# Kernel optimization log

Measured on AMD Instinct MI355X. Metric: run time of the kernel, lower is better.

## Reference

```python
import jax, jax.numpy as jnp
import numpy as np

N_NODES = 50000
N_EDGES = 800000
D = 128
E_DIM = 32
N_LAYERS = 4
BN_EPS = 1e-5


def setup_inputs() -> dict:
    key = jax.random.key(0)
    ks = jax.random.split(key, 9)
    return {
        "x": jax.random.normal(ks[0], (N_NODES, D), dtype=jnp.float32),
        "edge_attr": jax.random.normal(ks[1], (N_EDGES, E_DIM), dtype=jnp.float32),
        "edge_index": jax.random.randint(ks[2], (2, N_EDGES), 0, N_NODES, dtype=jnp.int64),
        "W_edge": jax.random.normal(ks[3], (N_LAYERS, E_DIM, D), dtype=jnp.float32) * 0.1,
        "b_edge": jnp.zeros((N_LAYERS, D), dtype=jnp.float32),
        "W1": jax.random.normal(ks[4], (N_LAYERS, D, D), dtype=jnp.float32) * 0.1,
        "b1": jnp.zeros((N_LAYERS, D), dtype=jnp.float32),
        "W2": jax.random.normal(ks[5], (N_LAYERS, D, D), dtype=jnp.float32) * 0.1,
        "b2": jnp.zeros((N_LAYERS, D), dtype=jnp.float32),
        "gamma": jnp.ones((N_LAYERS, D), dtype=jnp.float32),
        "beta": jnp.zeros((N_LAYERS, D), dtype=jnp.float32),
    }


def reference(x, edge_attr, edge_index, W_edge, b_edge, W1, b1, W2, b2, gamma, beta):
    src, dst = edge_index[0], edge_index[1]
    n = x.shape[0]
    for i in range(N_LAYERS):
        # GINEConv: message = ReLU(x_src + Lin(edge_attr)); scatter-add to dst
        e = edge_attr @ W_edge[i] + b_edge[i]            # [E, D]
        m = jax.nn.relu(x[src] + e)                      # [E, D]
        agg = jax.ops.segment_sum(m, dst, num_segments=n)  # [N, D]
        h = x + agg                                      # (1+eps)*x, eps=0
        # 2-layer MLP
        h = jax.nn.relu(h @ W1[i] + b1[i]) @ W2[i] + b2[i]
        # BatchNorm (training-mode batch stats, biased var) + ReLU; dropout off
        mean = h.mean(axis=0)
        var = h.var(axis=0)
        h = (h - mean) * jax.lax.rsqrt(var + BN_EPS) * gamma[i] + beta[i]
        x = jax.nn.relu(h)
    return x
```

## Files before the change

### kernel.cpp

```cpp
#include <hip/hip_runtime.h>

#define NN 50000
#define NE 800000
#define DD 128
#define ED 32
#define NL 4
#define BN_EPS 1e-5f
#define SCAN_B 1024
#define NB ((NN + SCAN_B - 1) / SCAN_B)
#define EB 128
#define MR 32

typedef __attribute__((ext_vector_type(8))) short bf16x8;
typedef __attribute__((ext_vector_type(4))) float f32x4;

__device__ __forceinline__ unsigned short f2bf(float f) {
    unsigned u = __float_as_uint(f);
    u += 0x7fffu + ((u >> 16) & 1u);
    return (unsigned short)(u >> 16);
}
__device__ __forceinline__ float bf2f(unsigned short h) {
    return __uint_as_float((unsigned)h << 16);
}

__global__ __launch_bounds__(256) void hist_kernel(
    const int* __restrict__ edst, int* __restrict__ deg)
{
    const int e = blockIdx.x * 256 + threadIdx.x;
    if (e < NE) atomicAdd(&deg[edst[e]], 1);
}

__global__ __launch_bounds__(256) void scan1_kernel(
    const int* __restrict__ deg, int* __restrict__ rowptr, int* __restrict__ bsum)
{
    __shared__ int sh[256];
    const int t = threadIdx.x, b = blockIdx.x;
    const int base = b * SCAN_B + t * 4;
    int v[4];
#pragma unroll
    for (int j = 0; j < 4; ++j) {
        const int idx = base + j;
        v[j] = (idx < NN) ? deg[idx] : 0;
    }
    sh[t] = v[0] + v[1] + v[2] + v[3];
    __syncthreads();
    for (int off = 1; off < 256; off <<= 1) {
        const int val = (t >= off) ? sh[t - off] : 0;
        __syncthreads();
        sh[t] += val;
        __syncthreads();
    }
    int p = (t == 0) ? 0 : sh[t - 1];
#pragma unroll
    for (int j = 0; j < 4; ++j) {
        const int idx = base + j;
        if (idx < NN) rowptr[idx] = p;
        p += v[j];
    }
    if (t == 255) bsum[b] = sh[255];
}

__global__ void scan2_kernel(int* __restrict__ bsum)
{
    if (threadIdx.x == 0) {
        int acc = 0;
        for (int i = 0; i < NB; ++i) { const int v = bsum[i]; bsum[i] = acc; acc += v; }
    }
}

__global__ __launch_bounds__(256) void scan3_kernel(
    int* __restrict__ rowptr, int* __restrict__ cursor, const int* __restrict__ bsum)
{
    const int idx = blockIdx.x * 256 + threadIdx.x;
    if (idx < NN) {
        const int v = rowptr[idx] + bsum[idx / SCAN_B];
        rowptr[idx] = v;
        cursor[idx] = v;
    }
    if (idx == 0) rowptr[NN] = NE;
}

__global__ __launch_bounds__(256) void scatter_idx_kernel(
    const int* __restrict__ esrc, const int* __restrict__ edst,
    int* __restrict__ cursor, int2* __restrict__ sd_perm, int* __restrict__ eid_perm)
{
    const int e = blockIdx.x * 256 + threadIdx.x;
    if (e < NE) {
        const int d = edst[e];
        const int pos = atomicAdd(&cursor[d], 1);
        sd_perm[pos] = make_int2(esrc[e], d);
        eid_perm[pos] = e;
    }
}

__global__ __launch_bounds__(256) void ea_gather_kernel(
    const float* __restrict__ ea, const int* __restrict__ eid_perm,
    unsigned short* __restrict__ ea_bf)
{
    const int tid = blockIdx.x * 256 + threadIdx.x;
    const int pos = tid >> 3, j = tid & 7;
    if (pos < NE) {
        const int e = eid_perm[pos];
        const float4 v = *(const float4*)&ea[(size_t)e * ED + j * 4];
        uint2 p;
        p.x = (unsigned)f2bf(v.x) | ((unsigned)f2bf(v.y) << 16);
        p.y = (unsigned)f2bf(v.z) | ((unsigned)f2bf(v.w) << 16);
        *(uint2*)&ea_bf[(size_t)pos * ED + j * 4] = p;
    }
}

__global__ __launch_bounds__(256) void x0conv_kernel(
    const float* __restrict__ x0, unsigned short* __restrict__ xbf)
{
    const size_t i = ((size_t)blockIdx.x * 256 + threadIdx.x) * 8;
    if (i >= (size_t)NN * DD) return;
    const float4 a = *(const float4*)&x0[i];
    const float4 b = *(const float4*)&x0[i + 4];
    uint4 o;
    o.x = (unsigned)f2bf(a.x) | ((unsigned)f2bf(a.y) << 16);
    o.y = (unsigned)f2bf(a.z) | ((unsigned)f2bf(a.w) << 16);
    o.z = (unsigned)f2bf(b.x) | ((unsigned)f2bf(b.y) << 16);
    o.w = (unsigned)f2bf(b.z) | ((unsigned)f2bf(b.w) << 16);
    *(uint4*)&xbf[i] = o;
}

__global__ __launch_bounds__(256) void wconv_kernel(
    const float* __restrict__ We, unsigned short* __restrict__ wtb)
{
    const int tid = blockIdx.x * 256 + threadIdx.x;
    if (tid < NL * DD * ED) {
        const int l = tid / (DD * ED);
        const int r = tid % (DD * ED);
        const int c = r / ED, k = r % ED;
        wtb[tid] = f2bf(We[(size_t)l * ED * DD + k * DD + c]);
    }
}

__global__ __launch_bounds__(256) void w12conv_kernel(
    const float* __restrict__ W1, const float* __restrict__ W2,
    unsigned short* __restrict__ w1t, unsigned short* __restrict__ w2t)
{
    const int tid = blockIdx.x * 256 + threadIdx.x;
    if (tid < NL * DD * DD) {
        const int l = tid / (DD * DD);
        const int r = tid % (DD * DD);
        const int n = r / DD, k = r % DD;
        const size_t s = (size_t)l * DD * DD + k * DD + n;
        w1t[tid] = f2bf(W1[s]);
        w2t[tid] = f2bf(W2[s]);
    }
}

__global__ __launch_bounds__(256, 5) void edge_mfma_kernel(
    const unsigned short* __restrict__ xbf,
    const unsigned short* __restrict__ eab,
    const int2* __restrict__ sd_perm,
    const unsigned short* __restrict__ wtb,
    const float* __restrict__ be,
    float* __restrict__ agg)
{
    __shared__ unsigned short msgl[EB * 128];
    const int t = threadIdx.x;
    const int wv = t >> 6, ln = t & 63;
    const int l15 = ln & 15, kb = ln >> 4;
    const int e0 = blockIdx.x * EB;

    const int c0 = (2 * wv + 0) * 16 + l15;
    const int c1 = (2 * wv + 1) * 16 + l15;
    const bf16x8 bfr0 = *(const bf16x8*)&wtb[c0 * ED + kb * 8];
    const bf16x8 bfr1 = *(const bf16x8*)&wtb[c1 * ED + kb * 8];

#pragma unroll
    for (int eg = 0; eg < EB / 16; ++eg) {
        const int edge = eg * 16 + l15;
        const bf16x8 afr = *(const bf16x8*)&eab[(size_t)(e0 + edge) * ED + kb * 8];
        f32x4 z = {0.f, 0.f, 0.f, 0.f};
        const f32x4 d0 = __builtin_amdgcn_mfma_f32_16x16x32_bf16(afr, bfr0, z, 0, 0, 0);
        const f32x4 d1 = __builtin_amdgcn_mfma_f32_16x16x32_bf16(afr, bfr1, z, 0, 0, 0);
#pragma unroll
        for (int j = 0; j < 4; ++j) {
            const int mrow = eg * 16 + kb * 4 + j;
            const int sw = ((mrow >> 2) & 3) << 3;
            const int i0 = (((c0 >> 1) ^ sw) << 1) | (c0 & 1);
            const int i1 = (((c1 >> 1) ^ sw) << 1) | (c1 & 1);
            msgl[mrow * 128 + i0] = f2bf(d0[j]);
            msgl[mrow * 128 + i1] = f2bf(d1[j]);
        }
    }
    __syncthreads();

    const int lbase = wv * 32;
    const int2* sdp = &sd_perm[e0 + lbase];
    const int c2 = ln * 2;
    const float2 bv = *(const float2*)&be[c2];
    float2 acc = {0.f, 0.f};
    int seg_start = 0;
#pragma unroll 1
    for (int g = 0; g < 4; ++g) {
        const int gb = g * 8;
        int4 pr[4];
#pragma unroll
        for (int q = 0; q < 4; ++q)
            pr[q] = *(const int4*)&sdp[gb + 2 * q];
        const int srcs[8] = {pr[0].x, pr[0].z, pr[1].x, pr[1].z,
                             pr[2].x, pr[2].z, pr[3].x, pr[3].z};
        int dsts[9];
        dsts[0] = pr[0].y; dsts[1] = pr[0].w; dsts[2] = pr[1].y; dsts[3] = pr[1].w;
        dsts[4] = pr[2].y; dsts[5] = pr[2].w; dsts[6] = pr[3].y; dsts[7] = pr[3].w;
        dsts[8] = (gb + 8 < 32) ? sdp[gb + 8].y : -1;
        float2 xv[8];
#pragma unroll
        for (int q = 0; q < 8; ++q) {
            const unsigned xu = *(const unsigned*)&xbf[(size_t)srcs[q] * DD + c2];
            xv[q].x = __uint_as_float(xu << 16);
            xv[q].y = __uint_as_float(xu & 0xffff0000u);
        }
#pragma unroll
        for (int q = 0; q < 8; ++q) {
            const int i = gb + q;
            const int dw = ln ^ (((i >> 2) & 3) << 3);
            const unsigned mm = *(const unsigned*)&msgl[(lbase + i) * 128 + dw * 2];
            const float mlo = __uint_as_float(mm << 16);
            const float mhi = __uint_as_float(mm & 0xffff0000u);
            acc.x += fmaxf(xv[q].x + mlo + bv.x, 0.f);
            acc.y += fmaxf(xv[q].y + mhi + bv.y, 0.f);
            if (i == 31 || dsts[q + 1] != dsts[q]) {
                float* ap = &agg[(size_t)dsts[q] * DD + c2];
                if (seg_start > 0 && i < 31) {
                    *(float2*)ap = acc;
                } else {
                    unsafeAtomicAdd(ap + 0, acc.x);
                    unsafeAtomicAdd(ap + 1, acc.y);
                }
                acc.x = 0.f; acc.y = 0.f;
                seg_start = i + 1;
            }
        }
    }
}

__global__ __launch_bounds__(256, 5) void mlp_mfma_kernel(
    const unsigned short* __restrict__ xbf, const float* __restrict__ agg,
    float* __restrict__ h2out,
    const unsigned short* __restrict__ w1t,
    const unsigned short* __restrict__ w2t,
    const float* __restrict__ b1, const float* __restrict__ b2,
    float* __restrict__ bns)
{
    __shared__ unsigned short ah[MR * 128];
    __shared__ unsigned short al[MR * 128];
    __shared__ unsigned short bh[MR * 128];
    __shared__ unsigned short bl[MR * 128];
    const int t = threadIdx.x;
    const int wv = t >> 6, ln = t & 63, l15 = ln & 15, kb = ln >> 4;
    const int r0 = blockIdx.x * MR;

#pragma unroll
    for (int p = 0; p < 2; ++p) {
        const int row = p * 16 + (t >> 4);
        const int gc = t & 15;
        const int grow = r0 + row;
        float v[8] = {0.f, 0.f, 0.f, 0.f, 0.f, 0.f, 0.f, 0.f};
        if (grow < NN) {
            const size_t g = (size_t)grow * DD + gc * 8;
            const uint4 xu = *(const uint4*)&xbf[g];
            const float4 ga = *(const float4*)&agg[g];
            const float4 gb4 = *(const float4*)&agg[g + 4];
            v[0] = __uint_as_float(xu.x << 16)          + ga.x;
            v[1] = __uint_as_float(xu.x & 0xffff0000u)  + ga.y;
            v[2] = __uint_as_float(xu.y << 16)          + ga.z;
            v[3] = __uint_as_float(xu.y & 0xffff0000u)  + ga.w;
            v[4] = __uint_as_float(xu.z << 16)          + gb4.x;
            v[5] = __uint_as_float(xu.z & 0xffff0000u)  + gb4.y;
            v[6] = __uint_as_float(xu.w << 16)          + gb4.z;
            v[7] = __uint_as_float(xu.w & 0xffff0000u)  + gb4.w;
        }
        unsigned hiw[4], low[4];
#pragma unroll
        for (int j = 0; j < 4; ++j) {
            const unsigned short h0 = f2bf(v[2 * j]);
            const unsigned short h1 = f2bf(v[2 * j + 1]);
            const unsigned short q0 = f2bf(v[2 * j] - bf2f(h0));
            const unsigned short q1 = f2bf(v[2 * j + 1] - bf2f(h1));
            hiw[j] = (unsigned)h0 | ((unsigned)h1 << 16);
            low[j] = (unsigned)q0 | ((unsigned)q1 << 16);
        }
        const int off = row * 128 + (gc ^ (row & 7)) * 8;
        *(uint4*)&ah[off] = *(uint4*)hiw;
        *(uint4*)&al[off] = *(uint4*)low;
    }

    bf16x8 w1f[2][4];
#pragma unroll
    for (int nt = 0; nt < 2; ++nt) {
        const int n = wv * 32 + nt * 16 + l15;
#pragma unroll
        for (int ks = 0; ks < 4; ++ks)
            w1f[nt][ks] = *(const bf16x8*)&w1t[n * DD + ks * 32 + kb * 8];
    }
    const int cA = wv * 32 + l15, cB = wv * 32 + 16 + l15;
    const float b1v[2] = {b1[cA], b1[cB]};
    const float b2v[2] = {b2[cA], b2[cB]};
    __syncthreads();

    f32x4 acc[2][2];
#pragma unroll
    for (int mt = 0; mt < 2; ++mt)
#pragma unroll
        for (int nt = 0; nt < 2; ++nt)
            acc[mt][nt] = (f32x4){0.f, 0.f, 0.f, 0.f};
#pragma unroll
    for (int ks = 0; ks < 4; ++ks) {
#pragma unroll
        for (int mt = 0; mt < 2; ++mt) {
            const int row = mt * 16 + l15;
            const int off = row * 128 + ((ks * 4 + kb) ^ (row & 7)) * 8;
            const bf16x8 afh = *(const bf16x8*)&ah[off];
            const bf16x8 afl = *(const bf16x8*)&al[off];
#pragma unroll
            for (int nt = 0; nt < 2; ++nt) {
                acc[mt][nt] = __builtin_amdgcn_mfma_f32_16x16x32_bf16(afh, w1f[nt][ks], acc[mt][nt], 0, 0, 0);
                acc[mt][nt] = __builtin_amdgcn_mfma_f32_16x16x32_bf16(afl, w1f[nt][ks], acc[mt][nt], 0, 0, 0);
            }
        }
    }

#pragma unroll
    for (int mt = 0; mt < 2; ++mt) {
#pragma unroll
        for (int nt = 0; nt < 2; ++nt) {
            const int col = wv * 32 + nt * 16 + l15;
#pragma unroll
            for (int j = 0; j < 4; ++j) {
                const int row = mt * 16 + kb * 4 + j;
                const float v = fmaxf(acc[mt][nt][j] + b1v[nt], 0.f);
                const unsigned short hi = f2bf(v);
                const int off = row * 128 + ((col >> 3) ^ (row & 7)) * 8 + (col & 7);
                bh[off] = hi;
                bl[off] = f2bf(v - bf2f(hi));
            }
        }
    }

    bf16x8 w2f[2][4];
#pragma unroll
    for (int nt = 0; nt < 2; ++nt) {
        const int n = wv * 32 + nt * 16 + l15;
#pragma unroll
        for (int ks = 0; ks < 4; ++ks)
            w2f[nt][ks] = *(const bf16x8*)&w2t[n * DD + ks * 32 + kb * 8];
    }
    __syncthreads();

#pragma unroll
    for (int mt = 0; mt < 2; ++mt)
#pragma unroll
        for (int nt = 0; nt < 2; ++nt)
            acc[mt][nt] = (f32x4){0.f, 0.f, 0.f, 0.f};
#pragma unroll
    for (int ks = 0; ks < 4; ++ks) {
#pragma unroll
        for (int mt = 0; mt < 2; ++mt) {
            const int row = mt * 16 + l15;
            const int off = row * 128 + ((ks * 4 + kb) ^ (row & 7)) * 8;
            const bf16x8 afh = *(const bf16x8*)&bh[off];
            const bf16x8 afl = *(const bf16x8*)&bl[off];
#pragma unroll
            for (int nt = 0; nt < 2; ++nt) {
                acc[mt][nt] = __builtin_amdgcn_mfma_f32_16x16x32_bf16(afh, w2f[nt][ks], acc[mt][nt], 0, 0, 0);
                acc[mt][nt] = __builtin_amdgcn_mfma_f32_16x16x32_bf16(afl, w2f[nt][ks], acc[mt][nt], 0, 0, 0);
            }
        }
    }

    float ps[2] = {0.f, 0.f}, pq[2] = {0.f, 0.f};
#pragma unroll
    for (int mt = 0; mt < 2; ++mt) {
#pragma unroll
        for (int nt = 0; nt < 2; ++nt) {
            const int col = wv * 32 + nt * 16 + l15;
#pragma unroll
            for (int j = 0; j < 4; ++j) {
                const int row = r0 + mt * 16 + kb * 4 + j;
                const float v = acc[mt][nt][j] + b2v[nt];
                if (row < NN) {
                    h2out[(size_t)row * DD + col] = v;
                    ps[nt] += v;
                    pq[nt] += v * v;
                }
            }
        }
    }
#pragma unroll
    for (int nt = 0; nt < 2; ++nt) {
        ps[nt] += __shfl_xor(ps[nt], 16);
        ps[nt] += __shfl_xor(ps[nt], 32);
        pq[nt] += __shfl_xor(pq[nt], 16);
        pq[nt] += __shfl_xor(pq[nt], 32);
    }
    if (kb == 0) {
#pragma unroll
        for (int nt = 0; nt < 2; ++nt) {
            const int col = wv * 32 + nt * 16 + l15;
            unsafeAtomicAdd(&bns[col], ps[nt]);
            unsafeAtomicAdd(&bns[DD + col], pq[nt]);
        }
    }
}

__global__ __launch_bounds__(256) void bn_apply_bf16(
    const float* __restrict__ h2, const float* __restrict__ bns,
    const float* __restrict__ gamma, const float* __restrict__ beta,
    unsigned short* __restrict__ xout)
{
    const size_t i = ((size_t)blockIdx.x * 256 + threadIdx.x) * 4;
    if (i >= (size_t)NN * DD) return;
    const int c4 = (int)(i & 127);
    const float4 hv = *(const float4*)&h2[i];
    const float4 sv = *(const float4*)&bns[c4];
    const float4 qv = *(const float4*)&bns[DD + c4];
    const float4 gv = *(const float4*)&gamma[c4];
    const float4 bv = *(const float4*)&beta[c4];
    const float inv_n = 1.f / (float)NN;
    float o0, o1, o2, o3;
    { const float m = sv.x * inv_n; const float var = qv.x * inv_n - m * m;
      o0 = fmaxf((hv.x - m) * __frsqrt_rn(var + BN_EPS) * gv.x + bv.x, 0.f); }
    { const float m = sv.y * inv_n; const float var = qv.y * inv_n - m * m;
      o1 = fmaxf((hv.y - m) * __frsqrt_rn(var + BN_EPS) * gv.y + bv.y, 0.f); }
    { const float m = sv.z * inv_n; const float var = qv.z * inv_n - m * m;
      o2 = fmaxf((hv.z - m) * __frsqrt_rn(var + BN_EPS) * gv.z + bv.z, 0.f); }
    { const float m = sv.w * inv_n; const float var = qv.w * inv_n - m * m;
      o3 = fmaxf((hv.w - m) * __frsqrt_rn(var + BN_EPS) * gv.w + bv.w, 0.f); }
    uint2 o;
    o.x = (unsigned)f2bf(o0) | ((unsigned)f2bf(o1) << 16);
    o.y = (unsigned)f2bf(o2) | ((unsigned)f2bf(o3) << 16);
    *(uint2*)&xout[i] = o;
}

__global__ __launch_bounds__(256) void bn_apply_f32(
    const float* __restrict__ h2, const float* __restrict__ bns,
    const float* __restrict__ gamma, const float* __restrict__ beta,
    float* __restrict__ xout)
{
    const size_t i = ((size_t)blockIdx.x * 256 + threadIdx.x) * 4;
    if (i >= (size_t)NN * DD) return;
    const int c4 = (int)(i & 127);
    const float4 hv = *(const float4*)&h2[i];
    const float4 sv = *(const float4*)&bns[c4];
    const float4 qv = *(const float4*)&bns[DD + c4];
    const float4 gv = *(const float4*)&gamma[c4];
    const float4 bv = *(const float4*)&beta[c4];
    const float inv_n = 1.f / (float)NN;
    float4 ov;
    { const float m = sv.x * inv_n; const float var = qv.x * inv_n - m * m;
      ov.x = fmaxf((hv.x - m) * __frsqrt_rn(var + BN_EPS) * gv.x + bv.x, 0.f); }
    { const float m = sv.y * inv_n; const float var = qv.y * inv_n - m * m;
      ov.y = fmaxf((hv.y - m) * __frsqrt_rn(var + BN_EPS) * gv.y + bv.y, 0.f); }
    { const float m = sv.z * inv_n; const float var = qv.z * inv_n - m * m;
      ov.z = fmaxf((hv.z - m) * __frsqrt_rn(var + BN_EPS) * gv.z + bv.z, 0.f); }
    { const float m = sv.w * inv_n; const float var = qv.w * inv_n - m * m;
      ov.w = fmaxf((hv.w - m) * __frsqrt_rn(var + BN_EPS) * gv.w + bv.w, 0.f); }
    *(float4*)&xout[i] = ov;
}

extern "C" void kernel_launch(void* const* d_in, const int* in_sizes, int n_in,
                              void* d_out, int out_size, void* d_ws, size_t ws_size,
                              hipStream_t stream) {
    const float* x0    = (const float*)d_in[0];
    const float* ea    = (const float*)d_in[1];
    const int*   eidx  = (const int*)d_in[2];
    const float* We    = (const float*)d_in[3];
    const float* be    = (const float*)d_in[4];
    const float* W1    = (const float*)d_in[5];
    const float* b1    = (const float*)d_in[6];
    const float* W2    = (const float*)d_in[7];
    const float* b2    = (const float*)d_in[8];
    const float* gamma = (const float*)d_in[9];
    const float* beta  = (const float*)d_in[10];
    float* out = (float*)d_out;
    float* ws  = (float*)d_ws;

    float* agg = ws;
    float* bns = agg + (size_t)NN * DD;
    int* deg      = (int*)(bns + 256);
    int* rowptr   = deg + 50000;
    int* cursor   = rowptr + 50004;
    int* bsum     = cursor + 50000;
    int2* sd_perm = (int2*)(bsum + 64);
    int* eid_perm = (int*)(sd_perm + NE);
    unsigned short* ea_bf = (unsigned short*)(eid_perm + NE);
    unsigned short* wt_bf = ea_bf + (size_t)NE * ED;
    unsigned short* w1t   = wt_bf + (size_t)NL * DD * ED;
    unsigned short* w2t   = w1t + (size_t)NL * DD * DD;
    unsigned short* xbf   = w2t + (size_t)NL * DD * DD;

    const int* esrc = eidx;
    const int* edst = eidx + NE;

    hipMemsetAsync(deg, 0, NN * sizeof(int), stream);
    hist_kernel<<<(NE + 255) / 256, 256, 0, stream>>>(edst, deg);
    scan1_kernel<<<NB, 256, 0, stream>>>(deg, rowptr, bsum);
    scan2_kernel<<<1, 64, 0, stream>>>(bsum);
    scan3_kernel<<<(NN + 255) / 256, 256, 0, stream>>>(rowptr, cursor, bsum);
    scatter_idx_kernel<<<(NE + 255) / 256, 256, 0, stream>>>(
        esrc, edst, cursor, sd_perm, eid_perm);
    ea_gather_kernel<<<(NE * 8 + 255) / 256, 256, 0, stream>>>(ea, eid_perm, ea_bf);
    x0conv_kernel<<<((NN * DD / 8) + 255) / 256, 256, 0, stream>>>(x0, xbf);
    wconv_kernel<<<(NL * DD * ED + 255) / 256, 256, 0, stream>>>(We, wt_bf);
    w12conv_kernel<<<(NL * DD * DD + 255) / 256, 256, 0, stream>>>(W1, W2, w1t, w2t);

    for (int l = 0; l < NL; ++l) {
        hipMemsetAsync(agg, 0, (size_t)NN * DD * sizeof(float), stream);
        hipMemsetAsync(bns, 0, 2 * DD * sizeof(float), stream);
        edge_mfma_kernel<<<NE / EB, 256, 0, stream>>>(
            xbf, ea_bf, sd_perm,
            wt_bf + (size_t)l * DD * ED, be + (size_t)l * DD, agg);
        mlp_mfma_kernel<<<(NN + MR - 1) / MR, 256, 0, stream>>>(
            xbf, agg, agg,
            w1t + (size_t)l * DD * DD, w2t + (size_t)l * DD * DD,
            b1 + (size_t)l * DD, b2 + (size_t)l * DD, bns);
        if (l < NL - 1) {
            bn_apply_bf16<<<(NN * DD / 4 + 255) / 256, 256, 0, stream>>>(
                agg, bns, gamma + (size_t)l * DD, beta + (size_t)l * DD, xbf);
        } else {
            bn_apply_f32<<<(NN * DD / 4 + 255) / 256, 256, 0, stream>>>(
                agg, bns, gamma + (size_t)l * DD, beta + (size_t)l * DD, out);
        }
    }
}
```

Before: 669.7 us.

## Fold agg zeroing into BN apply, deterministic sd_perm fill, wider gather batches

The per-layer memset of the aggregation buffer is replaced by having bn_apply_bf16 write zeros back to h2 after reading it, and the BN stats get one slot per layer so they are cleared once up front. The scatter kernel now only writes eid_perm; a new per-node kernel fills sd_perm from rowptr so its writes are sequential. The edge kernel gathers 16 source rows per batch instead of 8 to put more loads in flight. The costs are one extra small kernel launch, a serial per-node loop in sdfill, and higher register pressure in the edge kernel.

```diff
diff --git a/kernel.cpp b/kernel.cpp
--- a/kernel.cpp
+++ b/kernel.cpp
@@ -81,15 +81,24 @@
 }
 
 __global__ __launch_bounds__(256) void scatter_idx_kernel(
-    const int* __restrict__ esrc, const int* __restrict__ edst,
-    int* __restrict__ cursor, int2* __restrict__ sd_perm, int* __restrict__ eid_perm)
+    const int* __restrict__ edst, int* __restrict__ cursor, int* __restrict__ eid_perm)
 {
     const int e = blockIdx.x * 256 + threadIdx.x;
     if (e < NE) {
-        const int d = edst[e];
-        const int pos = atomicAdd(&cursor[d], 1);
-        sd_perm[pos] = make_int2(esrc[e], d);
+        const int pos = atomicAdd(&cursor[edst[e]], 1);
         eid_perm[pos] = e;
+    }
+}
+
+__global__ __launch_bounds__(256) void sdfill_kernel(
+    const int* __restrict__ rowptr, const int* __restrict__ eid_perm,
+    const int* __restrict__ esrc, int2* __restrict__ sd_perm)
+{
+    const int d = blockIdx.x * 256 + threadIdx.x;
+    if (d < NN) {
+        const int b = rowptr[d], e = rowptr[d + 1];
+        for (int p = b; p < e; ++p)
+            sd_perm[p] = make_int2(esrc[eid_perm[p]], d);
     }
 }
 
@@ -196,27 +205,28 @@
     float2 acc = {0.f, 0.f};
     int seg_start = 0;
 #pragma unroll 1
-    for (int g = 0; g < 4; ++g) {
-        const int gb = g * 8;
-        int4 pr[4];
-#pragma unroll
-        for (int q = 0; q < 4; ++q)
+    for (int g = 0; g < 2; ++g) {
+        const int gb = g * 16;
+        int4 pr[8];
+#pragma unroll
+        for (int q = 0; q < 8; ++q)
             pr[q] = *(const int4*)&sdp[gb + 2 * q];
-        const int srcs[8] = {pr[0].x, pr[0].z, pr[1].x, pr[1].z,
-                             pr[2].x, pr[2].z, pr[3].x, pr[3].z};
-        int dsts[9];
-        dsts[0] = pr[0].y; dsts[1] = pr[0].w; dsts[2] = pr[1].y; dsts[3] = pr[1].w;
-        dsts[4] = pr[2].y; dsts[5] = pr[2].w; dsts[6] = pr[3].y; dsts[7] = pr[3].w;
-        dsts[8] = (gb + 8 < 32) ? sdp[gb + 8].y : -1;
-        float2 xv[8];
+        int srcs[16], dsts[17];
 #pragma unroll
         for (int q = 0; q < 8; ++q) {
+            srcs[2 * q] = pr[q].x; srcs[2 * q + 1] = pr[q].z;
+            dsts[2 * q] = pr[q].y; dsts[2 * q + 1] = pr[q].w;
+        }
+        dsts[16] = (gb + 16 < 32) ? sdp[gb + 16].y : -1;
+        float2 xv[16];
+#pragma unroll
+        for (int q = 0; q < 16; ++q) {
             const unsigned xu = *(const unsigned*)&xbf[(size_t)srcs[q] * DD + c2];
             xv[q].x = __uint_as_float(xu << 16);
             xv[q].y = __uint_as_float(xu & 0xffff0000u);
         }
 #pragma unroll
-        for (int q = 0; q < 8; ++q) {
+        for (int q = 0; q < 16; ++q) {
             const int i = gb + q;
             const int dw = ln ^ (((i >> 2) & 3) << 3);
             const unsigned mm = *(const unsigned*)&msgl[(lbase + i) * 128 + dw * 2];
@@ -409,7 +419,7 @@
 }
 
 __global__ __launch_bounds__(256) void bn_apply_bf16(
-    const float* __restrict__ h2, const float* __restrict__ bns,
+    float* __restrict__ h2, const float* __restrict__ bns,
     const float* __restrict__ gamma, const float* __restrict__ beta,
     unsigned short* __restrict__ xout)
 {
@@ -435,6 +445,7 @@
     o.x = (unsigned)f2bf(o0) | ((unsigned)f2bf(o1) << 16);
     o.y = (unsigned)f2bf(o2) | ((unsigned)f2bf(o3) << 16);
     *(uint2*)&xout[i] = o;
+    *(float4*)&h2[i] = (float4){0.f, 0.f, 0.f, 0.f};
 }
 
 __global__ __launch_bounds__(256) void bn_apply_f32(
@@ -482,7 +493,7 @@
 
     float* agg = ws;
     float* bns = agg + (size_t)NN * DD;
-    int* deg      = (int*)(bns + 256);
+    int* deg      = (int*)(bns + NL * 256);
     int* rowptr   = deg + 50000;
     int* cursor   = rowptr + 50004;
     int* bsum     = cursor + 50000;
@@ -498,33 +509,33 @@
     const int* edst = eidx + NE;
 
     hipMemsetAsync(deg, 0, NN * sizeof(int), stream);
+    hipMemsetAsync(bns, 0, NL * 256 * sizeof(float), stream);
+    hipMemsetAsync(agg, 0, (size_t)NN * DD * sizeof(float), stream);
     hist_kernel<<<(NE + 255) / 256, 256, 0, stream>>>(edst, deg);
     scan1_kernel<<<NB, 256, 0, stream>>>(deg, rowptr, bsum);
     scan2_kernel<<<1, 64, 0, stream>>>(bsum);
     scan3_kernel<<<(NN + 255) / 256, 256, 0, stream>>>(rowptr, cursor, bsum);
-    scatter_idx_kernel<<<(NE + 255) / 256, 256, 0, stream>>>(
-        esrc, edst, cursor, sd_perm, eid_perm);
+    scatter_idx_kernel<<<(NE + 255) / 256, 256, 0, stream>>>(edst, cursor, eid_perm);
+    sdfill_kernel<<<(NN + 255) / 256, 256, 0, stream>>>(rowptr, eid_perm, esrc, sd_perm);
     ea_gather_kernel<<<(NE * 8 + 255) / 256, 256, 0, stream>>>(ea, eid_perm, ea_bf);
     x0conv_kernel<<<((NN * DD / 8) + 255) / 256, 256, 0, stream>>>(x0, xbf);
     wconv_kernel<<<(NL * DD * ED + 255) / 256, 256, 0, stream>>>(We, wt_bf);
     w12conv_kernel<<<(NL * DD * DD + 255) / 256, 256, 0, stream>>>(W1, W2, w1t, w2t);
 
     for (int l = 0; l < NL; ++l) {
-        hipMemsetAsync(agg, 0, (size_t)NN * DD * sizeof(float), stream);
-        hipMemsetAsync(bns, 0, 2 * DD * sizeof(float), stream);
         edge_mfma_kernel<<<NE / EB, 256, 0, stream>>>(
             xbf, ea_bf, sd_perm,
             wt_bf + (size_t)l * DD * ED, be + (size_t)l * DD, agg);
         mlp_mfma_kernel<<<(NN + MR - 1) / MR, 256, 0, stream>>>(
             xbf, agg, agg,
             w1t + (size_t)l * DD * DD, w2t + (size_t)l * DD * DD,
-            b1 + (size_t)l * DD, b2 + (size_t)l * DD, bns);
+            b1 + (size_t)l * DD, b2 + (size_t)l * DD, bns + l * 256);
         if (l < NL - 1) {
             bn_apply_bf16<<<(NN * DD / 4 + 255) / 256, 256, 0, stream>>>(
-                agg, bns, gamma + (size_t)l * DD, beta + (size_t)l * DD, xbf);
+                agg, bns + l * 256, gamma + (size_t)l * DD, beta + (size_t)l * DD, xbf);
         } else {
             bn_apply_f32<<<(NN * DD / 4 + 255) / 256, 256, 0, stream>>>(
-                agg, bns, gamma + (size_t)l * DD, beta + (size_t)l * DD, out);
-        }
-    }
-}
+                agg, bns + l * 256, gamma + (size_t)l * DD, beta + (size_t)l * DD, out);
+        }
+    }
+}
```

Result: faster. 650.3 us (-2.9%).
